# Optimization experiments

Measured on AMD Instinct MI355X. Metric: run time of the kernel, lower is better.

Reference implementation:

```python
import jax, jax.numpy as jnp
import numpy as np

D_K = 64  # module-level constant in source
NEG = -1e9


def setup_inputs() -> dict:
    key = jax.random.key(0)
    k1, k2, k3, k4 = jax.random.split(key, 4)
    B, H, S, D = 4, 16, 2048, 64
    query = jax.random.normal(k1, (B, H, S, D), dtype=jnp.float32)
    key_t = jax.random.normal(k2, (B, H, S, D), dtype=jnp.float32)
    value = jax.random.normal(k3, (B, H, S, D), dtype=jnp.float32)
    mask = jax.random.randint(k4, (B, 1, S, S), 0, 2) == 1  # bool, broadcast over heads
    return {"query": query, "key": key_t, "value": value, "mask": mask}


def reference(query, key, value, mask):
    # scores = QK^T / sqrt(d_k)   [B,H,S,S]
    scores = jnp.einsum("bhqd,bhkd->bhqk", query, key) / jnp.sqrt(jnp.float32(D_K))
    # masked_fill_(mask, -1e9)
    scores = jnp.where(mask, jnp.float32(NEG), scores)
    # non-standard: multiply masked scores by V, then log_softmax over last dim
    out = jnp.einsum("bhqk,bhkd->bhqd", scores, value)  # [B,H,S,d_v]
    return jax.nn.log_softmax(out, axis=-1)
```

## Files before the change

kernel.cpp:

```cpp
#include <hip/hip_runtime.h>
#include <hip/hip_bf16.h>


typedef __attribute__((ext_vector_type(8))) short bf16x8;
typedef __attribute__((ext_vector_type(16))) float f32x16;

#define NEGV (-1e9f)

__device__ inline unsigned cvt_bf16(float f) {
    unsigned u = __builtin_bit_cast(unsigned, f);
    u += 0x7FFFu + ((u >> 16) & 1u);
    return u >> 16;
}
__device__ inline unsigned pk_bf16(float a, float b) {
    return cvt_bf16(a) | (cvt_bf16(b) << 16);
}
__device__ inline unsigned pk_trunc(float a, float b) {
    return __builtin_amdgcn_perm(__builtin_bit_cast(unsigned, b),
                                 __builtin_bit_cast(unsigned, a), 0x07060302u);
}

__global__ __launch_bounds__(256)
void mask_pack(const int* __restrict__ M, unsigned long long* __restrict__ bitT) {
    const int lane = threadIdx.x & 63;
    const int gw   = (blockIdx.x * 256 + threadIdx.x) >> 6;
    const int nw   = (gridDim.x * 256) >> 6;
    for (int w = gw; w < 4 * 8 * 32 * 256; w += nw) {
        const int q  = w & 255;
        const int ki = (w >> 8) & 31;
        const int qt = (w >> 13) & 7;
        const int b  = w >> 16;
        const int m  = M[((size_t)(b * 2048 + qt * 256 + q)) * 2048 + ki * 64 + lane];
        const unsigned long long bal = __ballot(m != 0);
        if (lane == 0) bitT[w] = bal;
    }
}

__global__ __launch_bounds__(256, 3)
void attn_kernel(const float* __restrict__ Q, const float* __restrict__ K,
                 const float* __restrict__ V,
                 const unsigned long long* __restrict__ bitT,
                 float* __restrict__ Out) {
    __shared__ __attribute__((aligned(16))) unsigned short sK[2][64 * 72];
    __shared__ __attribute__((aligned(16))) unsigned short sVt[2][64 * 72];

    const int tid  = threadIdx.x;
    const int wave = tid >> 6;
    const int lane = tid & 63;
    const int half = lane >> 5;
    const int l32  = lane & 31;

    const int bid = blockIdx.x;
    const int h  = bid & 15;
    const int qt = (bid >> 4) & 7;
    const int b  = bid >> 7;
    const int bh = b * 16 + h;
    const int q0 = qt * 256;

    const float* Qb = Q + (size_t)(bh * 2048 + q0) * 64;
    const float* Kb = K + (size_t)bh * 2048 * 64;
    const float* Vb = V + (size_t)bh * 2048 * 64;
    const unsigned long long* Bt = bitT + (size_t)(b * 8 + qt) * 32 * 256
                                 + wave * 64 + half * 32 + l32;

    float4 kp[4];
    float  vp[16];
    unsigned long long mw = Bt[0];
    const int krow = tid >> 4, kc4 = tid & 15;
#pragma unroll
    for (int i = 0; i < 4; i++)
        kp[i] = *(const float4*)(Kb + (size_t)(krow + i * 16) * 64 + kc4 * 4);
#pragma unroll
    for (int i = 0; i < 2; i++) {
        const int kb = (wave * 2 + i) * 8;
#pragma unroll
        for (int j = 0; j < 8; j++)
            vp[i * 8 + j] = Vb[(size_t)(kb + j) * 64 + lane];
    }

    bf16x8 qF[2][4];
#pragma unroll
    for (int qb = 0; qb < 2; qb++) {
        const float* qr = Qb + (size_t)(wave * 64 + qb * 32 + l32) * 64 + half * 8;
#pragma unroll
        for (int dk = 0; dk < 4; dk++) {
            const float4 f0 = *(const float4*)(qr + dk * 16);
            const float4 f1 = *(const float4*)(qr + dk * 16 + 4);
            union { bf16x8 v; unsigned u[4]; } t;
            t.u[0] = pk_bf16(f0.x * 0.125f, f0.y * 0.125f);
            t.u[1] = pk_bf16(f0.z * 0.125f, f0.w * 0.125f);
            t.u[2] = pk_bf16(f1.x * 0.125f, f1.y * 0.125f);
            t.u[3] = pk_bf16(f1.z * 0.125f, f1.w * 0.125f);
            qF[qb][dk] = t.v;
        }
    }

    f32x16 Oacc[2][2];
#pragma unroll
    for (int qb = 0; qb < 2; qb++)
#pragma unroll
        for (int db = 0; db < 2; db++)
#pragma unroll
            for (int r = 0; r < 16; r++) Oacc[qb][db][r] = 0.f;

    for (int ki = 0; ki < 32; ki++) {
        const int cur = ki & 1;

#pragma unroll
        for (int i = 0; i < 4; i++) {
            uint2 p;
            p.x = pk_trunc(kp[i].x, kp[i].y);
            p.y = pk_trunc(kp[i].z, kp[i].w);
            *(uint2*)&sK[cur][(krow + i * 16) * 72 + kc4 * 4] = p;
        }
#pragma unroll
        for (int i = 0; i < 2; i++) {
            const int kb = (wave * 2 + i) * 8;
            uint4 p4;
            p4.x = pk_bf16(vp[i * 8 + 0], vp[i * 8 + 1]);
            p4.y = pk_bf16(vp[i * 8 + 2], vp[i * 8 + 3]);
            p4.z = pk_bf16(vp[i * 8 + 4], vp[i * 8 + 5]);
            p4.w = pk_bf16(vp[i * 8 + 6], vp[i * 8 + 7]);
            *(uint4*)&sVt[cur][lane * 72 + kb] = p4;
        }

        __syncthreads();

        unsigned long long mwN = 0;
        if (ki < 31) {
            const int kn = (ki + 1) * 64;
            mwN = Bt[(ki + 1) * 256];
#pragma unroll
            for (int i = 0; i < 4; i++)
                kp[i] = *(const float4*)(Kb + (size_t)(kn + krow + i * 16) * 64 + kc4 * 4);
#pragma unroll
            for (int i = 0; i < 2; i++) {
                const int kb = (wave * 2 + i) * 8;
#pragma unroll
                for (int j = 0; j < 8; j++)
                    vp[i * 8 + j] = Vb[(size_t)(kn + kb + j) * 64 + lane];
            }
        }

        unsigned w0lo, w1lo, w0hi, w1hi;
        {
            union { unsigned long long v; unsigned u[2]; } mu; mu.v = mw;
            auto rlo = __builtin_amdgcn_permlane32_swap(mu.u[0], mu.u[0], false, false);
            auto rhi = __builtin_amdgcn_permlane32_swap(mu.u[1], mu.u[1], false, false);
            w0lo = rlo[0]; w1lo = rlo[1];
            w0hi = rhi[0]; w1hi = rhi[1];
        }

#pragma unroll
        for (int jk = 0; jk < 2; jk++) {
            bf16x8 aK[4];
#pragma unroll
            for (int dk = 0; dk < 4; dk++)
                aK[dk] = *(const bf16x8*)&sK[cur][(jk * 32 + l32) * 72 + dk * 16 + half * 8];
            bf16x8 bV[2][2];
#pragma unroll
            for (int p = 0; p < 2; p++)
#pragma unroll
                for (int db = 0; db < 2; db++)
                    bV[p][db] = *(const bf16x8*)&sVt[cur][(db * 32 + l32) * 72 + (jk * 2 + p) * 16 + half * 8];

#pragma unroll
            for (int qb = 0; qb < 2; qb++) {
                const unsigned b32 = jk ? (qb ? w1hi : w0hi) : (qb ? w1lo : w0lo);
                const unsigned bsh = b32 >> (half * 4);

                f32x16 acc;
#pragma unroll
                for (int rg = 0; rg < 4; rg++) {
                    const unsigned nib = bsh >> (rg * 8);
                    acc[rg * 4 + 0] = (nib & 1u) ? NEGV : 0.f;
                    acc[rg * 4 + 1] = (nib & 2u) ? NEGV : 0.f;
                    acc[rg * 4 + 2] = (nib & 4u) ? NEGV : 0.f;
                    acc[rg * 4 + 3] = (nib & 8u) ? NEGV : 0.f;
                }
#pragma unroll
                for (int dk = 0; dk < 4; dk++)
                    acc = __builtin_amdgcn_mfma_f32_32x32x16_bf16(aK[dk], qF[qb][dk], acc, 0, 0, 0);

#pragma unroll
                for (int p = 0; p < 2; p++) {
                    const unsigned P0 = pk_trunc(acc[p * 8 + 0], acc[p * 8 + 1]);
                    const unsigned P1 = pk_trunc(acc[p * 8 + 2], acc[p * 8 + 3]);
                    const unsigned P2 = pk_trunc(acc[p * 8 + 4], acc[p * 8 + 5]);
                    const unsigned P3 = pk_trunc(acc[p * 8 + 6], acc[p * 8 + 7]);
                    auto r02 = __builtin_amdgcn_permlane32_swap(P0, P2, false, false);
                    auto r13 = __builtin_amdgcn_permlane32_swap(P1, P3, false, false);
                    union { bf16x8 v; unsigned u[4]; } aS;
                    aS.u[0] = (unsigned)r02[0];
                    aS.u[1] = (unsigned)r13[0];
                    aS.u[2] = (unsigned)r02[1];
                    aS.u[3] = (unsigned)r13[1];
#pragma unroll
                    for (int db = 0; db < 2; db++)
                        Oacc[qb][db] = __builtin_amdgcn_mfma_f32_32x32x16_bf16(aS.v, bV[p][db], Oacc[qb][db], 0, 0, 0);
                }
            }
        }

        mw = mwN;
    }

    float* Ob = Out + (size_t)bh * 2048 * 64;
#pragma unroll
    for (int qb = 0; qb < 2; qb++) {
#pragma unroll
        for (int r = 0; r < 16; r++) {
            const float v0 = Oacc[qb][0][r], v1 = Oacc[qb][1][r];
            float mx = fmaxf(v0, v1);
#pragma unroll
            for (int off = 1; off < 32; off <<= 1)
                mx = fmaxf(mx, __shfl_xor(mx, off, 64));
            float s = __expf(v0 - mx) + __expf(v1 - mx);
#pragma unroll
            for (int off = 1; off < 32; off <<= 1)
                s += __shfl_xor(s, off, 64);
            const float lse = mx + __logf(s);
            const int qrow = q0 + wave * 64 + qb * 32 + (r & 3) + 8 * (r >> 2) + 4 * half;
            Ob[(size_t)qrow * 64 + l32]      = v0 - lse;
            Ob[(size_t)qrow * 64 + 32 + l32] = v1 - lse;
        }
    }
}

extern "C" void kernel_launch(void* const* d_in, const int* in_sizes, int n_in,
                              void* d_out, int out_size, void* d_ws, size_t ws_size,
                              hipStream_t stream) {
    const float* Q = (const float*)d_in[0];
    const float* K = (const float*)d_in[1];
    const float* V = (const float*)d_in[2];
    const int*   M = (const int*)d_in[3];
    float* Out = (float*)d_out;
    unsigned long long* bitT = (unsigned long long*)d_ws;

    mask_pack<<<dim3(4096), dim3(256), 0, stream>>>(M, bitT);
    attn_kernel<<<dim3(512), dim3(256), 0, stream>>>(Q, K, V, bitT, Out);
}
```

Measured before the change: 262.0 us.

## Halve query tile per block to 128 rows and double grid size

Each block now covers 128 query rows instead of 256, so every wave owns a single 32-row query block and the grid doubles to 1024 blocks. Per-wave accumulators and Q fragments shrink, the permlane mask shuffle is dropped because each lane reads its own mask word directly, and launch bounds go from 3 to 4 blocks per CU. The aim is better occupancy and more blocks across the 256 CUs, at the cost of loading and converting K/V tiles into shared memory twice as often per query row.

```diff
diff --git a/kernel.cpp b/kernel.cpp
--- a/kernel.cpp
+++ b/kernel.cpp
@@ -36,7 +36,7 @@
     }
 }
 
-__global__ __launch_bounds__(256, 3)
+__global__ __launch_bounds__(256, 4)
 void attn_kernel(const float* __restrict__ Q, const float* __restrict__ K,
                  const float* __restrict__ V,
                  const unsigned long long* __restrict__ bitT,
@@ -51,17 +51,19 @@
     const int l32  = lane & 31;
 
     const int bid = blockIdx.x;
-    const int h  = bid & 15;
-    const int qt = (bid >> 4) & 7;
-    const int b  = bid >> 7;
-    const int bh = b * 16 + h;
-    const int q0 = qt * 256;
+    const int h   = bid & 15;
+    const int qt2 = (bid >> 4) & 15;
+    const int b   = bid >> 8;
+    const int bh  = b * 16 + h;
+    const int q0  = qt2 * 128;
+    const int qt  = qt2 >> 1;
+    const int qh  = qt2 & 1;
 
     const float* Qb = Q + (size_t)(bh * 2048 + q0) * 64;
     const float* Kb = K + (size_t)bh * 2048 * 64;
     const float* Vb = V + (size_t)bh * 2048 * 64;
     const unsigned long long* Bt = bitT + (size_t)(b * 8 + qt) * 32 * 256
-                                 + wave * 64 + half * 32 + l32;
+                                 + qh * 128 + wave * 32 + l32;
 
     float4 kp[4];
     float  vp[16];
@@ -78,10 +80,9 @@
             vp[i * 8 + j] = Vb[(size_t)(kb + j) * 64 + lane];
     }
 
-    bf16x8 qF[2][4];
-#pragma unroll
-    for (int qb = 0; qb < 2; qb++) {
-        const float* qr = Qb + (size_t)(wave * 64 + qb * 32 + l32) * 64 + half * 8;
+    bf16x8 qF[4];
+    {
+        const float* qr = Qb + (size_t)(wave * 32 + l32) * 64 + half * 8;
 #pragma unroll
         for (int dk = 0; dk < 4; dk++) {
             const float4 f0 = *(const float4*)(qr + dk * 16);
@@ -91,17 +92,15 @@
             t.u[1] = pk_bf16(f0.z * 0.125f, f0.w * 0.125f);
             t.u[2] = pk_bf16(f1.x * 0.125f, f1.y * 0.125f);
             t.u[3] = pk_bf16(f1.z * 0.125f, f1.w * 0.125f);
-            qF[qb][dk] = t.v;
-        }
-    }
-
-    f32x16 Oacc[2][2];
-#pragma unroll
-    for (int qb = 0; qb < 2; qb++)
-#pragma unroll
-        for (int db = 0; db < 2; db++)
-#pragma unroll
-            for (int r = 0; r < 16; r++) Oacc[qb][db][r] = 0.f;
+            qF[dk] = t.v;
+        }
+    }
+
+    f32x16 Oacc[2];
+#pragma unroll
+    for (int db = 0; db < 2; db++)
+#pragma unroll
+        for (int r = 0; r < 16; r++) Oacc[db][r] = 0.f;
 
     for (int ki = 0; ki < 32; ki++) {
         const int cur = ki & 1;
@@ -142,15 +141,6 @@
             }
         }
 
-        unsigned w0lo, w1lo, w0hi, w1hi;
-        {
-            union { unsigned long long v; unsigned u[2]; } mu; mu.v = mw;
-            auto rlo = __builtin_amdgcn_permlane32_swap(mu.u[0], mu.u[0], false, false);
-            auto rhi = __builtin_amdgcn_permlane32_swap(mu.u[1], mu.u[1], false, false);
-            w0lo = rlo[0]; w1lo = rlo[1];
-            w0hi = rhi[0]; w1hi = rhi[1];
-        }
-
 #pragma unroll
         for (int jk = 0; jk < 2; jk++) {
             bf16x8 aK[4];
@@ -164,42 +154,39 @@
                 for (int db = 0; db < 2; db++)
                     bV[p][db] = *(const bf16x8*)&sVt[cur][(db * 32 + l32) * 72 + (jk * 2 + p) * 16 + half * 8];
 
-#pragma unroll
-            for (int qb = 0; qb < 2; qb++) {
-                const unsigned b32 = jk ? (qb ? w1hi : w0hi) : (qb ? w1lo : w0lo);
-                const unsigned bsh = b32 >> (half * 4);
-
-                f32x16 acc;
-#pragma unroll
-                for (int rg = 0; rg < 4; rg++) {
-                    const unsigned nib = bsh >> (rg * 8);
-                    acc[rg * 4 + 0] = (nib & 1u) ? NEGV : 0.f;
-                    acc[rg * 4 + 1] = (nib & 2u) ? NEGV : 0.f;
-                    acc[rg * 4 + 2] = (nib & 4u) ? NEGV : 0.f;
-                    acc[rg * 4 + 3] = (nib & 8u) ? NEGV : 0.f;
-                }
-#pragma unroll
-                for (int dk = 0; dk < 4; dk++)
-                    acc = __builtin_amdgcn_mfma_f32_32x32x16_bf16(aK[dk], qF[qb][dk], acc, 0, 0, 0);
-
-#pragma unroll
-                for (int p = 0; p < 2; p++) {
-                    const unsigned P0 = pk_trunc(acc[p * 8 + 0], acc[p * 8 + 1]);
-                    const unsigned P1 = pk_trunc(acc[p * 8 + 2], acc[p * 8 + 3]);
-                    const unsigned P2 = pk_trunc(acc[p * 8 + 4], acc[p * 8 + 5]);
-                    const unsigned P3 = pk_trunc(acc[p * 8 + 6], acc[p * 8 + 7]);
-                    auto r02 = __builtin_amdgcn_permlane32_swap(P0, P2, false, false);
-                    auto r13 = __builtin_amdgcn_permlane32_swap(P1, P3, false, false);
-                    union { bf16x8 v; unsigned u[4]; } aS;
-                    aS.u[0] = (unsigned)r02[0];
-                    aS.u[1] = (unsigned)r13[0];
-                    aS.u[2] = (unsigned)r02[1];
-                    aS.u[3] = (unsigned)r13[1];
-#pragma unroll
-                    for (int db = 0; db < 2; db++)
-                        Oacc[qb][db] = __builtin_amdgcn_mfma_f32_32x32x16_bf16(aS.v, bV[p][db], Oacc[qb][db], 0, 0, 0);
-                }
+            const unsigned b32 = (unsigned)(mw >> (jk * 32));
+            const unsigned bsh = b32 >> (half * 4);
+
+            f32x16 acc;
+#pragma unroll
+            for (int rg = 0; rg < 4; rg++) {
+                const unsigned nib = bsh >> (rg * 8);
+                acc[rg * 4 + 0] = (nib & 1u) ? NEGV : 0.f;
+                acc[rg * 4 + 1] = (nib & 2u) ? NEGV : 0.f;
+                acc[rg * 4 + 2] = (nib & 4u) ? NEGV : 0.f;
+                acc[rg * 4 + 3] = (nib & 8u) ? NEGV : 0.f;
             }
+#pragma unroll
+            for (int dk = 0; dk < 4; dk++)
+                acc = __builtin_amdgcn_mfma_f32_32x32x16_bf16(aK[dk], qF[dk], acc, 0, 0, 0);
+
+#pragma unroll
+            for (int p = 0; p < 2; p++) {
+                const unsigned P0 = pk_trunc(acc[p * 8 + 0], acc[p * 8 + 1]);
+                const unsigned P1 = pk_trunc(acc[p * 8 + 2], acc[p * 8 + 3]);
+                const unsigned P2 = pk_trunc(acc[p * 8 + 4], acc[p * 8 + 5]);
+                const unsigned P3 = pk_trunc(acc[p * 8 + 6], acc[p * 8 + 7]);
+                auto r02 = __builtin_amdgcn_permlane32_swap(P0, P2, false, false);
+                auto r13 = __builtin_amdgcn_permlane32_swap(P1, P3, false, false);
+                union { bf16x8 v; unsigned u[4]; } aS;
+                aS.u[0] = (unsigned)r02[0];
+                aS.u[1] = (unsigned)r13[0];
+                aS.u[2] = (unsigned)r02[1];
+                aS.u[3] = (unsigned)r13[1];
+#pragma unroll
+                for (int db = 0; db < 2; db++)
+                    Oacc[db] = __builtin_amdgcn_mfma_f32_32x32x16_bf16(aS.v, bV[p][db], Oacc[db], 0, 0, 0);
+            }
         }
 
         mw = mwN;
@@ -207,23 +194,20 @@
 
     float* Ob = Out + (size_t)bh * 2048 * 64;
 #pragma unroll
-    for (int qb = 0; qb < 2; qb++) {
-#pragma unroll
-        for (int r = 0; r < 16; r++) {
-            const float v0 = Oacc[qb][0][r], v1 = Oacc[qb][1][r];
-            float mx = fmaxf(v0, v1);
-#pragma unroll
-            for (int off = 1; off < 32; off <<= 1)
-                mx = fmaxf(mx, __shfl_xor(mx, off, 64));
-            float s = __expf(v0 - mx) + __expf(v1 - mx);
-#pragma unroll
-            for (int off = 1; off < 32; off <<= 1)
-                s += __shfl_xor(s, off, 64);
-            const float lse = mx + __logf(s);
-            const int qrow = q0 + wave * 64 + qb * 32 + (r & 3) + 8 * (r >> 2) + 4 * half;
-            Ob[(size_t)qrow * 64 + l32]      = v0 - lse;
-            Ob[(size_t)qrow * 64 + 32 + l32] = v1 - lse;
-        }
+    for (int r = 0; r < 16; r++) {
+        const float v0 = Oacc[0][r], v1 = Oacc[1][r];
+        float mx = fmaxf(v0, v1);
+#pragma unroll
+        for (int off = 1; off < 32; off <<= 1)
+            mx = fmaxf(mx, __shfl_xor(mx, off, 64));
+        float s = __expf(v0 - mx) + __expf(v1 - mx);
+#pragma unroll
+        for (int off = 1; off < 32; off <<= 1)
+            s += __shfl_xor(s, off, 64);
+        const float lse = mx + __logf(s);
+        const int qrow = q0 + wave * 32 + (r & 3) + 8 * (r >> 2) + 4 * half;
+        Ob[(size_t)qrow * 64 + l32]      = v0 - lse;
+        Ob[(size_t)qrow * 64 + 32 + l32] = v1 - lse;
     }
 }
 
@@ -238,5 +222,5 @@
     unsigned long long* bitT = (unsigned long long*)d_ws;
 
     mask_pack<<<dim3(4096), dim3(256), 0, stream>>>(M, bitT);
-    attn_kernel<<<dim3(512), dim3(256), 0, stream>>>(Q, K, V, bitT, Out);
-}
+    attn_kernel<<<dim3(1024), dim3(256), 0, stream>>>(Q, K, V, bitT, Out);
+}
```

After: 265.4 us. No clear change (+1.3%).
